# Performance work log

Hardware: AMD Instinct MI355X
Metric: run time of the kernel (lower is better)

The kernel has to match this reference:

```python
import jax, jax.numpy as jnp
import numpy as np

B, N, C_IN, C_OUT, E_DIM = 16, 1024, 64, 64, 4


def setup_inputs() -> dict:
    key = jax.random.key(0)
    ks = jax.random.split(key, 7)
    x = jax.random.normal(ks[0], (B, N, C_IN), dtype=jnp.float32)
    adj = jax.random.uniform(ks[1], (B, N, N), dtype=jnp.float32)
    edge_attr = jax.random.randint(ks[2], (B, N, N, 1), 0, E_DIM, dtype=jnp.int32)
    scale = 1.0 / np.sqrt(C_IN)
    W_rel = jax.random.normal(ks[3], (C_IN, C_OUT), dtype=jnp.float32) * scale
    b_rel = jax.random.normal(ks[4], (C_OUT,), dtype=jnp.float32) * scale
    W_root = jax.random.normal(ks[5], (C_IN, C_OUT), dtype=jnp.float32) * scale
    w_edge = jax.random.normal(ks[6], (E_DIM,), dtype=jnp.float32)
    return {"x": x, "adj": adj, "edge_attr": edge_attr,
            "W_rel": W_rel, "b_rel": b_rel, "W_root": W_root, "w_edge": w_edge}


def reference(x, adj, edge_attr, W_rel, b_rel, W_root, w_edge):
    # one_hot(edge_attr) @ w_edge == gather of w_edge by edge type (same math,
    # avoids materializing the B x N x N x E_DIM one-hot tensor).
    e = w_edge[edge_attr[..., 0]]            # [B, N, N]
    adj_w = adj * e                           # weighted adjacency
    out = jnp.matmul(adj_w, x)                # [B, N, C_IN] aggregation (aggr='add')
    out = jnp.matmul(out, W_rel) + b_rel      # lin_rel
    out = out + jnp.matmul(x, W_root)         # lin_root (no bias)
    return out
```

## Files before the change

kernel.cpp:

```cpp
#include <hip/hip_runtime.h>

#define BB 16
#define NN 1024
#define CC 64

typedef __attribute__((ext_vector_type(8))) short short8;
typedef __attribute__((ext_vector_type(4))) float f32x4;

__device__ __forceinline__ unsigned short bf16_rne(float f) {
    unsigned u = __float_as_uint(f);
    u += 0x7fffu + ((u >> 16) & 1u);
    return (unsigned short)(u >> 16);
}

extern "C" __global__ __launch_bounds__(256)
void precompute(const float* __restrict__ x, const float* __restrict__ W_rel,
                const float* __restrict__ W_root, const float* __restrict__ b_rel,
                unsigned short* __restrict__ xw_sw, float* __restrict__ out)
{
    __shared__ float wrel_s[64 * 64];
    __shared__ float wroot_s[64 * 64];
    __shared__ float x_s[16 * 68];

    const int t = threadIdx.x;
    #pragma unroll
    for (int k = 0; k < 4; ++k) {
        int i4 = t + 256 * k;
        ((float4*)wrel_s)[i4]  = ((const float4*)W_rel)[i4];
        ((float4*)wroot_s)[i4] = ((const float4*)W_root)[i4];
    }
    const int row0 = blockIdx.x * 16;
    {
        int r = t >> 4, c4 = t & 15;
        *(float4*)(x_s + r * 68 + c4 * 4) = ((const float4*)(x + (size_t)(row0 + r) * CC))[c4];
    }
    __syncthreads();

    const int c4 = t & 15;
    const int r  = t >> 4;
    float aw0 = 0.f, aw1 = 0.f, aw2 = 0.f, aw3 = 0.f;
    float ar0 = 0.f, ar1 = 0.f, ar2 = 0.f, ar3 = 0.f;
    const float* xrow = x_s + r * 68;
    #pragma unroll 8
    for (int k = 0; k < 64; ++k) {
        float xv = xrow[k];
        float4 wv = ((const float4*)(wrel_s  + k * 64))[c4];
        float4 rv = ((const float4*)(wroot_s + k * 64))[c4];
        aw0 += xv * wv.x; aw1 += xv * wv.y; aw2 += xv * wv.z; aw3 += xv * wv.w;
        ar0 += xv * rv.x; ar1 += xv * rv.y; ar2 += xv * rv.z; ar3 += xv * rv.w;
    }

    const int row_g = row0 + r;
    {
        const float4 bv = ((const float4*)b_rel)[c4];
        ((float4*)out)[(size_t)row_g * 16 + c4] =
            make_float4(ar0 + bv.x, ar1 + bv.y, ar2 + bv.z, ar3 + bv.w);
    }
    {
        const int b = row_g >> 10;
        const int k = row_g & 1023;
        const int kb = k >> 5;
        const int qk = (k >> 3) & 3;
        const int j  = k & 7;
        const int c  = 4 * c4;
        const int n0 = c >> 4;
        const int n  = c & 15;
        size_t off = ((size_t)b << 16) + (size_t)((kb * 4 + n0) << 9)
                   + (size_t)((n + (qk << 4)) << 3) + j;
        xw_sw[off]      = bf16_rne(aw0);
        xw_sw[off + 8]  = bf16_rne(aw1);
        xw_sw[off + 16] = bf16_rne(aw2);
        xw_sw[off + 24] = bf16_rne(aw3);
    }
}

extern "C" __global__ __launch_bounds__(256, 6)
void gnn_mfma(const float* __restrict__ adj, const int* __restrict__ ea,
              const float* __restrict__ w_edge,
              const unsigned short* __restrict__ xw_sw,
              float* __restrict__ out)
{
    __shared__ float red_s[3 * 1088];

    const int t    = threadIdx.x;
    const int w    = t >> 6;
    const int lane = t & 63;
    const int m    = lane & 15;
    const int q    = lane >> 4;

    const int mtile = blockIdx.x & 63;
    const int khalf = (blockIdx.x >> 6) & 1;
    const int b     = blockIdx.x >> 7;

    const float w0 = w_edge[0], w1 = w_edge[1], w2 = w_edge[2], w3 = w_edge[3];
    const float d1 = w1 - w0;
    const float d2 = w2 - 2.f * w1 + w0;
    const float d3 = w3 - 3.f * w2 + 3.f * w1 - w0;
    const float c3 = d3 * (1.f / 6.f);
    const float c2 = 0.5f * d2 - 0.5f * d3;
    const float c1 = d1 - 0.5f * d2 + (1.f / 3.f) * d3;
    const float c0 = w0;

    const int row = (mtile << 4) + m;
    const size_t rowoff = (((size_t)b << 10) + row) * NN + (khalf << 9) + (w << 7) + (q << 3);
    const float* arow = adj + rowoff;
    const int*   erow = ea  + rowoff;
    const int kb0 = (khalf << 4) + (w << 2);
    const short8* xf = (const short8*)(xw_sw + ((size_t)b << 16)) + lane;

    f32x4 acc0 = {0.f, 0.f, 0.f, 0.f};
    f32x4 acc1 = acc0, acc2 = acc0, acc3 = acc0;

    #pragma unroll
    for (int kk = 0; kk < 4; ++kk) {
        const float* ap = arow + (kk << 5);
        const int*   ep = erow + (kk << 5);
        float4 a0 = *(const float4*)ap;
        float4 a1 = *(const float4*)(ap + 4);
        int4   e0 = *(const int4*)ep;
        int4   e1 = *(const int4*)(ep + 4);
        short8 bf0 = xf[((kb0 + kk) * 4 + 0) * 64];
        short8 bf1 = xf[((kb0 + kk) * 4 + 1) * 64];
        short8 bf2 = xf[((kb0 + kk) * 4 + 2) * 64];
        short8 bf3 = xf[((kb0 + kk) * 4 + 3) * 64];

        #define WSEL(ev) __builtin_fmaf(__builtin_fmaf(__builtin_fmaf(c3, (float)(ev), c2), (float)(ev), c1), (float)(ev), c0)
        float p0 = a0.x * WSEL(e0.x);
        float p1 = a0.y * WSEL(e0.y);
        float p2 = a0.z * WSEL(e0.z);
        float p3 = a0.w * WSEL(e0.w);
        float p4 = a1.x * WSEL(e1.x);
        float p5 = a1.y * WSEL(e1.y);
        float p6 = a1.z * WSEL(e1.z);
        float p7 = a1.w * WSEL(e1.w);
        #undef WSEL

        union { int i[4]; short8 s; } af;
        af.i[0] = __builtin_amdgcn_perm(__float_as_uint(p1), __float_as_uint(p0), 0x07060302u);
        af.i[1] = __builtin_amdgcn_perm(__float_as_uint(p3), __float_as_uint(p2), 0x07060302u);
        af.i[2] = __builtin_amdgcn_perm(__float_as_uint(p5), __float_as_uint(p4), 0x07060302u);
        af.i[3] = __builtin_amdgcn_perm(__float_as_uint(p7), __float_as_uint(p6), 0x07060302u);

        acc0 = __builtin_amdgcn_mfma_f32_16x16x32_bf16(af.s, bf0, acc0, 0, 0, 0);
        acc1 = __builtin_amdgcn_mfma_f32_16x16x32_bf16(af.s, bf1, acc1, 0, 0, 0);
        acc2 = __builtin_amdgcn_mfma_f32_16x16x32_bf16(af.s, bf2, acc2, 0, 0, 0);
        acc3 = __builtin_amdgcn_mfma_f32_16x16x32_bf16(af.s, bf3, acc3, 0, 0, 0);
    }

    if (w != 0) {
        float* buf = red_s + (w - 1) * 1088;
        #pragma unroll
        for (int rg = 0; rg < 4; ++rg) {
            int rbase = (q * 4 + rg) * 68 + m;
            buf[rbase]      = acc0[rg];
            buf[rbase + 16] = acc1[rg];
            buf[rbase + 32] = acc2[rg];
            buf[rbase + 48] = acc3[rg];
        }
    }
    __syncthreads();
    if (w == 0) {
        float* obase = out + (((size_t)b << 10) + (mtile << 4)) * 64;
        #pragma unroll
        for (int rg = 0; rg < 4; ++rg) {
            int rpad = (q * 4 + rg) * 68 + m;
            int rout = (q * 4 + rg) * 64 + m;
            #pragma unroll
            for (int n0 = 0; n0 < 4; ++n0) {
                int idx = rpad + n0 * 16;
                float v = (n0 == 0 ? acc0[rg] : n0 == 1 ? acc1[rg] : n0 == 2 ? acc2[rg] : acc3[rg]);
                v += red_s[idx] + red_s[1088 + idx] + red_s[2176 + idx];
                atomicAdd(obase + rout + n0 * 16, v);
            }
        }
    }
}

extern "C" void kernel_launch(void* const* d_in, const int* in_sizes, int n_in,
                              void* d_out, int out_size, void* d_ws, size_t ws_size,
                              hipStream_t stream) {
    const float* x      = (const float*)d_in[0];
    const float* adj    = (const float*)d_in[1];
    const int*   ea     = (const int*)  d_in[2];
    const float* W_rel  = (const float*)d_in[3];
    const float* b_rel  = (const float*)d_in[4];
    const float* W_root = (const float*)d_in[5];
    const float* w_edge = (const float*)d_in[6];
    float* out = (float*)d_out;

    unsigned short* xw_sw = (unsigned short*)d_ws;

    precompute<<<BB * NN / 16, 256, 0, stream>>>(x, W_rel, W_root, b_rel, xw_sw, out);
    gnn_mfma<<<BB * (NN / 16) * 2, 256, 0, stream>>>(adj, ea, w_edge, xw_sw, out);
}
```

Before: 175.6 us.

## Stage adj, edge and xw tiles into LDS via direct global-to-LDS loads

```diff
diff --git a/kernel.cpp b/kernel.cpp
--- a/kernel.cpp
+++ b/kernel.cpp
@@ -6,6 +6,14 @@
 
 typedef __attribute__((ext_vector_type(8))) short short8;
 typedef __attribute__((ext_vector_type(4))) float f32x4;
+typedef __attribute__((ext_vector_type(4))) int   i32x4;
+
+typedef __attribute__((address_space(3))) void lds_void_t;
+typedef const __attribute__((address_space(1))) void gbl_void_t;
+
+__device__ __forceinline__ void load_lds16(const void* g, void* l) {
+    __builtin_amdgcn_global_load_lds((gbl_void_t*)g, (lds_void_t*)l, 16, 0, 0);
+}
 
 __device__ __forceinline__ unsigned short bf16_rne(float f) {
     unsigned u = __float_as_uint(f);
@@ -74,23 +82,30 @@
     }
 }
 
-extern "C" __global__ __launch_bounds__(256, 6)
+#define ADJ_OFF 0
+#define EA_OFF  16384
+#define XW_OFF  32768
+
+extern "C" __global__ __launch_bounds__(256, 3)
 void gnn_mfma(const float* __restrict__ adj, const int* __restrict__ ea,
               const float* __restrict__ w_edge,
               const unsigned short* __restrict__ xw_sw,
               float* __restrict__ out)
 {
-    __shared__ float red_s[3 * 1088];
+    __shared__ __align__(16) char lds[49152];
 
     const int t    = threadIdx.x;
     const int w    = t >> 6;
     const int lane = t & 63;
     const int m    = lane & 15;
     const int q    = lane >> 4;
-
-    const int mtile = blockIdx.x & 63;
-    const int khalf = (blockIdx.x >> 6) & 1;
-    const int b     = blockIdx.x >> 7;
+    const int wm   = w >> 1;
+    const int wk   = w & 1;
+
+    const int mtile = blockIdx.x & 31;
+    const int kh    = (blockIdx.x >> 5) & 1;
+    const int b     = blockIdx.x >> 6;
+    const int row0  = mtile << 5;
 
     const float w0 = w_edge[0], w1 = w_edge[1], w2 = w_edge[2], w3 = w_edge[3];
     const float d1 = w1 - w0;
@@ -101,54 +116,80 @@
     const float c1 = d1 - 0.5f * d2 + (1.f / 3.f) * d3;
     const float c0 = w0;
 
-    const int row = (mtile << 4) + m;
-    const size_t rowoff = (((size_t)b << 10) + row) * NN + (khalf << 9) + (w << 7) + (q << 3);
-    const float* arow = adj + rowoff;
-    const int*   erow = ea  + rowoff;
-    const int kb0 = (khalf << 4) + (w << 2);
-    const short8* xf = (const short8*)(xw_sw + ((size_t)b << 16)) + lane;
+    const size_t bbase = ((size_t)b << 20);
+    const unsigned short* xwb = xw_sw + ((size_t)b << 16);
 
     f32x4 acc0 = {0.f, 0.f, 0.f, 0.f};
     f32x4 acc1 = acc0, acc2 = acc0, acc3 = acc0;
 
-    #pragma unroll
-    for (int kk = 0; kk < 4; ++kk) {
-        const float* ap = arow + (kk << 5);
-        const int*   ep = erow + (kk << 5);
-        float4 a0 = *(const float4*)ap;
-        float4 a1 = *(const float4*)(ap + 4);
-        int4   e0 = *(const int4*)ep;
-        int4   e1 = *(const int4*)(ep + 4);
-        short8 bf0 = xf[((kb0 + kk) * 4 + 0) * 64];
-        short8 bf1 = xf[((kb0 + kk) * 4 + 1) * 64];
-        short8 bf2 = xf[((kb0 + kk) * 4 + 2) * 64];
-        short8 bf3 = xf[((kb0 + kk) * 4 + 3) * 64];
-
-        #define WSEL(ev) __builtin_fmaf(__builtin_fmaf(__builtin_fmaf(c3, (float)(ev), c2), (float)(ev), c1), (float)(ev), c0)
-        float p0 = a0.x * WSEL(e0.x);
-        float p1 = a0.y * WSEL(e0.y);
-        float p2 = a0.z * WSEL(e0.z);
-        float p3 = a0.w * WSEL(e0.w);
-        float p4 = a1.x * WSEL(e1.x);
-        float p5 = a1.y * WSEL(e1.y);
-        float p6 = a1.z * WSEL(e1.z);
-        float p7 = a1.w * WSEL(e1.w);
-        #undef WSEL
-
-        union { int i[4]; short8 s; } af;
-        af.i[0] = __builtin_amdgcn_perm(__float_as_uint(p1), __float_as_uint(p0), 0x07060302u);
-        af.i[1] = __builtin_amdgcn_perm(__float_as_uint(p3), __float_as_uint(p2), 0x07060302u);
-        af.i[2] = __builtin_amdgcn_perm(__float_as_uint(p5), __float_as_uint(p4), 0x07060302u);
-        af.i[3] = __builtin_amdgcn_perm(__float_as_uint(p7), __float_as_uint(p6), 0x07060302u);
-
-        acc0 = __builtin_amdgcn_mfma_f32_16x16x32_bf16(af.s, bf0, acc0, 0, 0, 0);
-        acc1 = __builtin_amdgcn_mfma_f32_16x16x32_bf16(af.s, bf1, acc1, 0, 0, 0);
-        acc2 = __builtin_amdgcn_mfma_f32_16x16x32_bf16(af.s, bf2, acc2, 0, 0, 0);
-        acc3 = __builtin_amdgcn_mfma_f32_16x16x32_bf16(af.s, bf3, acc3, 0, 0, 0);
-    }
-
-    if (w != 0) {
-        float* buf = red_s + (w - 1) * 1088;
+    for (int c = 0; c < 4; ++c) {
+        const int kc = (kh << 9) + (c << 7);
+        if (c) __syncthreads();
+
+        #pragma unroll
+        for (int f = w; f < 16; f += 4) {
+            int mh = f >> 3;
+            int kb = (f >> 1) & 3;
+            int h  = f & 1;
+            int row = row0 + (mh << 4) + m;
+            int k   = kc + (kb << 5) + (q << 3) + (h << 2);
+            size_t goff = bbase + ((size_t)row << 10) + k;
+            int doff = ((mh * 4 + kb) << 11) + (h << 10);
+            load_lds16(adj + goff, lds + ADJ_OFF + doff);
+            load_lds16(ea  + goff, lds + EA_OFF  + doff);
+        }
+        #pragma unroll
+        for (int f = w; f < 16; f += 4) {
+            int kb = f >> 2, n0 = f & 3;
+            int kbg = (kh << 4) + (c << 2) + kb;
+            load_lds16(xwb + (((kbg << 2) + n0) << 9) + (lane << 3),
+                       lds + XW_OFF + (f << 10));
+        }
+        __syncthreads();
+
+        #pragma unroll
+        for (int s = 0; s < 2; ++s) {
+            int kb = (wk << 1) + s;
+            int fbase = ((wm * 4 + kb) << 11) + (lane << 4);
+            f32x4 alo = *(const f32x4*)(lds + ADJ_OFF + fbase);
+            f32x4 ahi = *(const f32x4*)(lds + ADJ_OFF + fbase + 1024);
+            i32x4 elo = *(const i32x4*)(lds + EA_OFF + fbase);
+            i32x4 ehi = *(const i32x4*)(lds + EA_OFF + fbase + 1024);
+
+            #define WSEL(ev) __builtin_fmaf(__builtin_fmaf(__builtin_fmaf(c3, (float)(ev), c2), (float)(ev), c1), (float)(ev), c0)
+            float p0 = alo[0] * WSEL(elo[0]);
+            float p1 = alo[1] * WSEL(elo[1]);
+            float p2 = alo[2] * WSEL(elo[2]);
+            float p3 = alo[3] * WSEL(elo[3]);
+            float p4 = ahi[0] * WSEL(ehi[0]);
+            float p5 = ahi[1] * WSEL(ehi[1]);
+            float p6 = ahi[2] * WSEL(ehi[2]);
+            float p7 = ahi[3] * WSEL(ehi[3]);
+            #undef WSEL
+
+            union { int i[4]; short8 s8; } af;
+            af.i[0] = __builtin_amdgcn_perm(__float_as_uint(p1), __float_as_uint(p0), 0x07060302u);
+            af.i[1] = __builtin_amdgcn_perm(__float_as_uint(p3), __float_as_uint(p2), 0x07060302u);
+            af.i[2] = __builtin_amdgcn_perm(__float_as_uint(p5), __float_as_uint(p4), 0x07060302u);
+            af.i[3] = __builtin_amdgcn_perm(__float_as_uint(p7), __float_as_uint(p6), 0x07060302u);
+
+            const char* xbase = lds + XW_OFF + ((kb << 2) << 10) + (lane << 4);
+            short8 bf0 = *(const short8*)(xbase);
+            short8 bf1 = *(const short8*)(xbase + 1024);
+            short8 bf2 = *(const short8*)(xbase + 2048);
+            short8 bf3 = *(const short8*)(xbase + 3072);
+
+            acc0 = __builtin_amdgcn_mfma_f32_16x16x32_bf16(af.s8, bf0, acc0, 0, 0, 0);
+            acc1 = __builtin_amdgcn_mfma_f32_16x16x32_bf16(af.s8, bf1, acc1, 0, 0, 0);
+            acc2 = __builtin_amdgcn_mfma_f32_16x16x32_bf16(af.s8, bf2, acc2, 0, 0, 0);
+            acc3 = __builtin_amdgcn_mfma_f32_16x16x32_bf16(af.s8, bf3, acc3, 0, 0, 0);
+        }
+    }
+
+    __syncthreads();
+    float* scratch = (float*)lds;
+    if (wk == 1) {
+        float* buf = scratch + wm * 1088;
         #pragma unroll
         for (int rg = 0; rg < 4; ++rg) {
             int rbase = (q * 4 + rg) * 68 + m;
@@ -159,17 +200,17 @@
         }
     }
     __syncthreads();
-    if (w == 0) {
-        float* obase = out + (((size_t)b << 10) + (mtile << 4)) * 64;
+    if (wk == 0) {
+        const float* buf = scratch + wm * 1088;
+        float* obase = out + (((size_t)b << 10) + row0 + (wm << 4)) * 64;
         #pragma unroll
         for (int rg = 0; rg < 4; ++rg) {
             int rpad = (q * 4 + rg) * 68 + m;
             int rout = (q * 4 + rg) * 64 + m;
             #pragma unroll
             for (int n0 = 0; n0 < 4; ++n0) {
-                int idx = rpad + n0 * 16;
                 float v = (n0 == 0 ? acc0[rg] : n0 == 1 ? acc1[rg] : n0 == 2 ? acc2[rg] : acc3[rg]);
-                v += red_s[idx] + red_s[1088 + idx] + red_s[2176 + idx];
+                v += buf[rpad + n0 * 16];
                 atomicAdd(obase + rout + n0 * 16, v);
             }
         }
@@ -191,5 +232,5 @@
     unsigned short* xw_sw = (unsigned short*)d_ws;
 
     precompute<<<BB * NN / 16, 256, 0, stream>>>(x, W_rel, W_root, b_rel, xw_sw, out);
-    gnn_mfma<<<BB * (NN / 16) * 2, 256, 0, stream>>>(adj, ea, w_edge, xw_sw, out);
-}
+    gnn_mfma<<<BB * (NN / 32) * 2, 256, 0, stream>>>(adj, ea, w_edge, xw_sw, out);
+}
```

Result: faster. 170.9 us (-2.7%).

## Stage per-batch XW panel in LDS with 1024-thread blocks over 64-row tiles

Applied to the files above, without the earlier changes.

```diff
diff --git a/kernel.cpp b/kernel.cpp
--- a/kernel.cpp
+++ b/kernel.cpp
@@ -6,6 +6,13 @@
 
 typedef __attribute__((ext_vector_type(8))) short short8;
 typedef __attribute__((ext_vector_type(4))) float f32x4;
+
+typedef __attribute__((address_space(3))) void lds_void_t;
+typedef const __attribute__((address_space(1))) void gbl_void_t;
+
+__device__ __forceinline__ void load_lds16(const void* g, void* l) {
+    __builtin_amdgcn_global_load_lds((gbl_void_t*)g, (lds_void_t*)l, 16, 0, 0);
+}
 
 __device__ __forceinline__ unsigned short bf16_rne(float f) {
     unsigned u = __float_as_uint(f);
@@ -74,23 +81,27 @@
     }
 }
 
-extern "C" __global__ __launch_bounds__(256, 6)
+extern "C" __global__ __launch_bounds__(1024, 4)
 void gnn_mfma(const float* __restrict__ adj, const int* __restrict__ ea,
               const float* __restrict__ w_edge,
               const unsigned short* __restrict__ xw_sw,
               float* __restrict__ out)
 {
-    __shared__ float red_s[3 * 1088];
+    __shared__ __align__(16) char lds[131072];
 
     const int t    = threadIdx.x;
     const int w    = t >> 6;
     const int lane = t & 63;
     const int m    = lane & 15;
     const int q    = lane >> 4;
-
-    const int mtile = blockIdx.x & 63;
-    const int khalf = (blockIdx.x >> 6) & 1;
-    const int b     = blockIdx.x >> 7;
+    const int wm   = w >> 2;
+    const int wk   = w & 3;
+
+    const int mt = blockIdx.x & 3;
+    const int mtile = blockIdx.x & 15;
+    const int b     = blockIdx.x >> 4;
+    const int row0  = mtile << 6;
+    (void)mt;
 
     const float w0 = w_edge[0], w1 = w_edge[1], w2 = w_edge[2], w3 = w_edge[3];
     const float d1 = w1 - w0;
@@ -101,54 +112,74 @@
     const float c1 = d1 - 0.5f * d2 + (1.f / 3.f) * d3;
     const float c0 = w0;
 
-    const int row = (mtile << 4) + m;
-    const size_t rowoff = (((size_t)b << 10) + row) * NN + (khalf << 9) + (w << 7) + (q << 3);
-    const float* arow = adj + rowoff;
-    const int*   erow = ea  + rowoff;
-    const int kb0 = (khalf << 4) + (w << 2);
-    const short8* xf = (const short8*)(xw_sw + ((size_t)b << 16)) + lane;
+    const int row = row0 + (wm << 4) + m;
+    const float* arow = adj + (((size_t)b << 10) + row) * NN;
+    const int*   erow = ea  + (((size_t)b << 10) + row) * NN;
+    const char*  xwb  = (const char*)xw_sw + ((size_t)b << 17);
+
+    #define STAGE_XW(p)                                                   \
+    {                                                                     \
+        _Pragma("unroll")                                                 \
+        for (int r = 0; r < 4; ++r) {                                     \
+            int off = ((p) << 16) + ((w * 4 + r) << 10) + (lane << 4);    \
+            load_lds16(xwb + off, lds + off);                             \
+        }                                                                 \
+    }
+
+    STAGE_XW(0);
+    __syncthreads();
+    STAGE_XW(1);
 
     f32x4 acc0 = {0.f, 0.f, 0.f, 0.f};
     f32x4 acc1 = acc0, acc2 = acc0, acc3 = acc0;
 
     #pragma unroll
-    for (int kk = 0; kk < 4; ++kk) {
-        const float* ap = arow + (kk << 5);
-        const int*   ep = erow + (kk << 5);
-        float4 a0 = *(const float4*)ap;
-        float4 a1 = *(const float4*)(ap + 4);
-        int4   e0 = *(const int4*)ep;
-        int4   e1 = *(const int4*)(ep + 4);
-        short8 bf0 = xf[((kb0 + kk) * 4 + 0) * 64];
-        short8 bf1 = xf[((kb0 + kk) * 4 + 1) * 64];
-        short8 bf2 = xf[((kb0 + kk) * 4 + 2) * 64];
-        short8 bf3 = xf[((kb0 + kk) * 4 + 3) * 64];
-
-        #define WSEL(ev) __builtin_fmaf(__builtin_fmaf(__builtin_fmaf(c3, (float)(ev), c2), (float)(ev), c1), (float)(ev), c0)
-        float p0 = a0.x * WSEL(e0.x);
-        float p1 = a0.y * WSEL(e0.y);
-        float p2 = a0.z * WSEL(e0.z);
-        float p3 = a0.w * WSEL(e0.w);
-        float p4 = a1.x * WSEL(e1.x);
-        float p5 = a1.y * WSEL(e1.y);
-        float p6 = a1.z * WSEL(e1.z);
-        float p7 = a1.w * WSEL(e1.w);
-        #undef WSEL
-
-        union { int i[4]; short8 s; } af;
-        af.i[0] = __builtin_amdgcn_perm(__float_as_uint(p1), __float_as_uint(p0), 0x07060302u);
-        af.i[1] = __builtin_amdgcn_perm(__float_as_uint(p3), __float_as_uint(p2), 0x07060302u);
-        af.i[2] = __builtin_amdgcn_perm(__float_as_uint(p5), __float_as_uint(p4), 0x07060302u);
-        af.i[3] = __builtin_amdgcn_perm(__float_as_uint(p7), __float_as_uint(p6), 0x07060302u);
-
-        acc0 = __builtin_amdgcn_mfma_f32_16x16x32_bf16(af.s, bf0, acc0, 0, 0, 0);
-        acc1 = __builtin_amdgcn_mfma_f32_16x16x32_bf16(af.s, bf1, acc1, 0, 0, 0);
-        acc2 = __builtin_amdgcn_mfma_f32_16x16x32_bf16(af.s, bf2, acc2, 0, 0, 0);
-        acc3 = __builtin_amdgcn_mfma_f32_16x16x32_bf16(af.s, bf3, acc3, 0, 0, 0);
-    }
-
-    if (w != 0) {
-        float* buf = red_s + (w - 1) * 1088;
+    for (int p = 0; p < 2; ++p) {
+        if (p) __syncthreads();
+        #pragma unroll
+        for (int kk = 0; kk < 4; ++kk) {
+            const int kbl = (wk << 2) + kk;
+            const int gk  = (p << 9) + (kbl << 5) + (q << 3);
+            float4 a0 = *(const float4*)(arow + gk);
+            float4 a1 = *(const float4*)(arow + gk + 4);
+            int4   e0 = *(const int4*)  (erow + gk);
+            int4   e1 = *(const int4*)  (erow + gk + 4);
+
+            const char* xbase = lds + (p << 16) + ((kbl << 2) << 10) + (lane << 4);
+            short8 bf0 = *(const short8*)(xbase);
+            short8 bf1 = *(const short8*)(xbase + 1024);
+            short8 bf2 = *(const short8*)(xbase + 2048);
+            short8 bf3 = *(const short8*)(xbase + 3072);
+
+            #define WSEL(ev) __builtin_fmaf(__builtin_fmaf(__builtin_fmaf(c3, (float)(ev), c2), (float)(ev), c1), (float)(ev), c0)
+            float p0 = a0.x * WSEL(e0.x);
+            float p1 = a0.y * WSEL(e0.y);
+            float p2 = a0.z * WSEL(e0.z);
+            float p3 = a0.w * WSEL(e0.w);
+            float p4 = a1.x * WSEL(e1.x);
+            float p5 = a1.y * WSEL(e1.y);
+            float p6 = a1.z * WSEL(e1.z);
+            float p7 = a1.w * WSEL(e1.w);
+            #undef WSEL
+
+            union { int i[4]; short8 s8; } af;
+            af.i[0] = __builtin_amdgcn_perm(__float_as_uint(p1), __float_as_uint(p0), 0x07060302u);
+            af.i[1] = __builtin_amdgcn_perm(__float_as_uint(p3), __float_as_uint(p2), 0x07060302u);
+            af.i[2] = __builtin_amdgcn_perm(__float_as_uint(p5), __float_as_uint(p4), 0x07060302u);
+            af.i[3] = __builtin_amdgcn_perm(__float_as_uint(p7), __float_as_uint(p6), 0x07060302u);
+
+            acc0 = __builtin_amdgcn_mfma_f32_16x16x32_bf16(af.s8, bf0, acc0, 0, 0, 0);
+            acc1 = __builtin_amdgcn_mfma_f32_16x16x32_bf16(af.s8, bf1, acc1, 0, 0, 0);
+            acc2 = __builtin_amdgcn_mfma_f32_16x16x32_bf16(af.s8, bf2, acc2, 0, 0, 0);
+            acc3 = __builtin_amdgcn_mfma_f32_16x16x32_bf16(af.s8, bf3, acc3, 0, 0, 0);
+        }
+    }
+    #undef STAGE_XW
+
+    __syncthreads();
+    float* scratch = (float*)lds;
+    if (wk != 0) {
+        float* buf = scratch + ((wk - 1) * 4 + wm) * 1088;
         #pragma unroll
         for (int rg = 0; rg < 4; ++rg) {
             int rbase = (q * 4 + rg) * 68 + m;
@@ -159,18 +190,20 @@
         }
     }
     __syncthreads();
-    if (w == 0) {
-        float* obase = out + (((size_t)b << 10) + (mtile << 4)) * 64;
+    if (wk == 0) {
+        const float* s1 = scratch + (0 * 4 + wm) * 1088;
+        const float* s2 = scratch + (1 * 4 + wm) * 1088;
+        const float* s3 = scratch + (2 * 4 + wm) * 1088;
+        float* obase = out + (((size_t)b << 10) + row0 + (wm << 4)) * 64;
         #pragma unroll
         for (int rg = 0; rg < 4; ++rg) {
             int rpad = (q * 4 + rg) * 68 + m;
             int rout = (q * 4 + rg) * 64 + m;
             #pragma unroll
             for (int n0 = 0; n0 < 4; ++n0) {
-                int idx = rpad + n0 * 16;
                 float v = (n0 == 0 ? acc0[rg] : n0 == 1 ? acc1[rg] : n0 == 2 ? acc2[rg] : acc3[rg]);
-                v += red_s[idx] + red_s[1088 + idx] + red_s[2176 + idx];
-                atomicAdd(obase + rout + n0 * 16, v);
+                v += s1[rpad + n0 * 16] + s2[rpad + n0 * 16] + s3[rpad + n0 * 16];
+                obase[rout + n0 * 16] += v;
             }
         }
     }
@@ -191,5 +224,5 @@
     unsigned short* xw_sw = (unsigned short*)d_ws;
 
     precompute<<<BB * NN / 16, 256, 0, stream>>>(x, W_rel, W_root, b_rel, xw_sw, out);
-    gnn_mfma<<<BB * (NN / 16) * 2, 256, 0, stream>>>(adj, ea, w_edge, xw_sw, out);
-}
+    gnn_mfma<<<BB * (NN / 64), 1024, 0, stream>>>(adj, ea, w_edge, xw_sw, out);
+}
```

After: 182.3 us. 3.8% more time.
